# Kernel optimization log

Measured on AMD Instinct MI355X. Metric: run time of the kernel, lower is better.

## Reference

```python
import jax, jax.numpy as jnp
import numpy as np

MODES = 32
NUM_BLOCKS = 4
NUM_EXPERTS = 16
TOP_K = 4
TEMPERATURE = 2.0


def _gelu(t):
    return jax.nn.gelu(t, approximate=False)  # torch F.gelu default (erf)


def _c1(x, w, b):
    # 1x1 conv: x [B,C,H,W], w [O,C], b [O]
    return jnp.einsum('bchw,oc->bohw', x, w) + b[None, :, None, None]


def _group_norm(x, w, b, groups=8, eps=1e-5):
    B, C, H, W = x.shape
    xg = x.reshape(B, groups, C // groups, H, W)
    mu = xg.mean(axis=(2, 3, 4), keepdims=True)
    var = xg.var(axis=(2, 3, 4), keepdims=True)
    xn = ((xg - mu) * jax.lax.rsqrt(var + eps)).reshape(B, C, H, W)
    return xn * w[None, :, None, None] + b[None, :, None, None]


def _bn_eval(x, g, b, rm, rv, eps=1e-5):
    # eval-mode BatchNorm with running stats
    return (x - rm) * jax.lax.rsqrt(rv + eps) * g + b


def _afno(x, w1, b1, w2, b2):
    # x: [B,C,H,W] (channel_first). Block-diagonal complex MLP on low FFT modes.
    B, C, H, W = x.shape
    bs = C // NUM_BLOCKS
    xp = x.transpose(0, 2, 3, 1)                      # [B,H,W,C]
    xf = jnp.fft.rfft2(xp, axes=(1, 2), norm='ortho') # [B,H,Wf,C] complex64
    Wf = xf.shape[2]
    xf = xf.reshape(B, H, Wf, NUM_BLOCKS, bs)
    m = MODES
    xm = xf[:, :m, :m]                                # kept modes only
    xr, xi = xm.real, xm.imag
    o1r = _gelu(jnp.einsum('bhwni,nio->bhwno', xr, w1[0])
                - jnp.einsum('bhwni,nio->bhwno', xi, w1[1]) + b1[0])
    o1i = _gelu(jnp.einsum('bhwni,nio->bhwno', xi, w1[0])
                + jnp.einsum('bhwni,nio->bhwno', xr, w1[1]) + b1[1])
    o2r = (jnp.einsum('bhwni,nio->bhwno', o1r, w2[0])
           - jnp.einsum('bhwni,nio->bhwno', o1i, w2[1]) + b2[0])
    o2i = (jnp.einsum('bhwni,nio->bhwno', o1i, w2[0])
           + jnp.einsum('bhwni,nio->bhwno', o1r, w2[1]) + b2[1])
    of = jnp.zeros((B, H, Wf, NUM_BLOCKS, bs), dtype=xf.dtype)
    of = of.at[:, :m, :m].set(o2r + 1j * o2i)
    out = jnp.fft.irfft2(of.reshape(B, H, Wf, C), s=(H, W), axes=(1, 2), norm='ortho')
    out = out + xp
    return out.transpose(0, 3, 1, 2)


def _forward(x, gn1_w, gn1_b, afno_w1, afno_b1, afno_w2, afno_b2,
             gn2_w, gn2_b, fe_w, fe_b, g1_w, g1_b, bn1_g, bn1_b, bn1_rm, bn1_rv,
             ca_w1, ca_b1, ca_w2, ca_b2, g2_w, g2_b, bn2_g, bn2_b, bn2_rm, bn2_rv,
             g3_w, g3_b, shared_w, shared_b, expert_w, expert_b):
    residual = x
    h = _group_norm(x, gn1_w, gn1_b)
    h = _afno(h, afno_w1, afno_b1, afno_w2, afno_b2)
    h = h + residual            # double_skip
    residual = h
    h = _group_norm(h, gn2_w, gn2_b)
    # MoEImage (eval mode -> loss_gate = 0)
    feats = _gelu(_c1(h, fe_w, fe_b))
    shared = jnp.zeros_like(h)
    for s in range(shared_w.shape[0]):
        shared = shared + _gelu(_c1(feats, shared_w[s], shared_b[s])) / shared_w.shape[0]
    # gating on global-avg-pooled features (1x1 convs == linears)
    gf = feats.mean(axis=(2, 3))                              # [B,C]
    h1 = _gelu(_bn_eval(gf @ g1_w.T + g1_b, bn1_g, bn1_b, bn1_rm, bn1_rv))
    a = _gelu(h1 @ ca_w1.T + ca_b1) @ ca_w2.T + ca_b2
    h1 = h1 * jax.nn.sigmoid(2.0 * a)                          # avg==max pool on 1x1 map
    h2 = _gelu(_bn_eval(h1 @ g2_w.T + g2_b, bn2_g, bn2_b, bn2_rm, bn2_rv))
    scores = h2 @ g3_w.T + g3_b                                # [B,E]
    vals, idx = jax.lax.top_k(scores, TOP_K)
    wts = jax.nn.softmax(vals / TEMPERATURE, axis=1)
    B = x.shape[0]
    gate_w = jnp.zeros((B, NUM_EXPERTS), x.dtype).at[jnp.arange(B)[:, None], idx].add(wts)
    out = shared
    for e in range(NUM_EXPERTS):
        out = out + _gelu(_c1(feats, expert_w[e], expert_b[e])) * gate_w[:, e][:, None, None, None]
    return out + residual


def setup_inputs():
    key = jax.random.key(0)
    ks = jax.random.split(key, 16)
    B, C, H, W = 8, 64, 192, 192
    nb = NUM_BLOCKS
    bs = C // nb
    E = NUM_EXPERTS
    scale = 1.0 / (bs * bs)
    f32 = jnp.float32
    n = lambda k, shape: jax.random.normal(k, shape, f32) * 0.02
    return {
        'x': jax.random.normal(ks[0], (B, C, H, W), f32),
        'gn1_w': jnp.ones((C,), f32), 'gn1_b': jnp.zeros((C,), f32),
        'afno_w1': jax.random.uniform(ks[1], (2, nb, bs, bs), f32) * scale,
        'afno_b1': jax.random.uniform(ks[2], (2, nb, bs), f32) * scale,
        'afno_w2': jax.random.uniform(ks[3], (2, nb, bs, bs), f32) * scale,
        'afno_b2': jax.random.uniform(ks[4], (2, nb, bs), f32) * scale,
        'gn2_w': jnp.ones((C,), f32), 'gn2_b': jnp.zeros((C,), f32),
        'fe_w': n(ks[5], (C, C)), 'fe_b': jnp.zeros((C,), f32),
        'g1_w': n(ks[6], (2 * C, C)), 'g1_b': jnp.zeros((2 * C,), f32),
        'bn1_g': jnp.ones((2 * C,), f32), 'bn1_b': jnp.zeros((2 * C,), f32),
        'bn1_rm': jnp.zeros((2 * C,), f32), 'bn1_rv': jnp.ones((2 * C,), f32),
        'ca_w1': n(ks[7], (2 * C // 16, 2 * C)), 'ca_b1': jnp.zeros((2 * C // 16,), f32),
        'ca_w2': n(ks[8], (2 * C, 2 * C // 16)), 'ca_b2': jnp.zeros((2 * C,), f32),
        'g2_w': n(ks[9], (C, 2 * C)), 'g2_b': jnp.zeros((C,), f32),
        'bn2_g': jnp.ones((C,), f32), 'bn2_b': jnp.zeros((C,), f32),
        'bn2_rm': jnp.zeros((C,), f32), 'bn2_rv': jnp.ones((C,), f32),
        'g3_w': n(ks[10], (E, C)), 'g3_b': jnp.zeros((E,), f32),
        'shared_w': n(ks[11], (2, C, C)), 'shared_b': jnp.zeros((2, C), f32),
        'expert_w': n(ks[12], (E, C, C)), 'expert_b': jnp.zeros((E, C), f32),
    }


def reference(x, gn1_w, gn1_b, afno_w1, afno_b1, afno_w2, afno_b2,
              gn2_w, gn2_b, fe_w, fe_b, g1_w, g1_b, bn1_g, bn1_b, bn1_rm, bn1_rv,
              ca_w1, ca_b1, ca_w2, ca_b2, g2_w, g2_b, bn2_g, bn2_b, bn2_rm, bn2_rv,
              g3_w, g3_b, shared_w, shared_b, expert_w, expert_b):
    return _forward(x, gn1_w, gn1_b, afno_w1, afno_b1, afno_w2, afno_b2,
                    gn2_w, gn2_b, fe_w, fe_b, g1_w, g1_b, bn1_g, bn1_b, bn1_rm, bn1_rv,
                    ca_w1, ca_b1, ca_w2, ca_b2, g2_w, g2_b, bn2_g, bn2_b, bn2_rm, bn2_rv,
                    g3_w, g3_b, shared_w, shared_b, expert_w, expert_b)
```

## Files before the change

### kernel.cpp

```cpp
#include <hip/hip_runtime.h>
#include <math.h>

#define TPI 6.283185307179586f

typedef __attribute__((ext_vector_type(8))) short bf8v;
typedef __attribute__((ext_vector_type(4))) float f4v;

#define MFMA(a,b,c) __builtin_amdgcn_mfma_f32_16x16x32_bf16((a),(b),(c),0,0,0)

__device__ __forceinline__ float gelu_f(float v){
  return 0.5f*v*(1.0f+erff(v*0.7071067811865475f));
}
__device__ __forceinline__ float gelu_fast(float x){
  float x2=x*x;
  float inner=fmaf(0.044715f*x2, x, x);
  float e=__expf(1.5957691216057308f*inner);
  float r=__builtin_amdgcn_rcpf(1.0f+e);
  return fmaf(-x, r, x);
}
__device__ __forceinline__ float gelu_sig(float x){
  float e=__expf(-1.702f*x);
  return x*__builtin_amdgcn_rcpf(1.0f+e);
}
__device__ __forceinline__ unsigned short f2b(float f){
  union{float f; unsigned u;} v; v.f=f;
  unsigned r=v.u + 0x7FFFu + ((v.u>>16)&1u);
  return (unsigned short)(r>>16);
}

__global__ __launch_bounds__(256) void prep(const float* __restrict__ shw, const float* __restrict__ exw,
    const float* __restrict__ shb, const float* __restrict__ exb, const float* __restrict__ few,
    unsigned short* __restrict__ T, unsigned short* __restrict__ wall, float* __restrict__ ball,
    unsigned short* __restrict__ wfe, float* __restrict__ gfp){
  const float a = TPI/192.0f;
  int stride=gridDim.x*256;
  for(int i=blockIdx.x*256+threadIdx.x; i<61440; i+=stride){
    float v;
    if(i<12288){
      int n1=i/192, w=i%192; int kw=n1>>1, c=n1&1;
      int m=(kw*w)%192; float cs,sn; sincosf((float)m*a,&sn,&cs);
      v = c ? -sn : cs;
    } else if(i<36864){
      int j=i-12288; int n1=j/384, k1=j%384; int kh=n1>>1, d=n1&1; int h=k1>>1, c=k1&1;
      int m=(kh*h)%192; float cs,sn; sincosf((float)m*a,&sn,&cs);
      float e = d ? (c ? cs : -sn) : (c ? sn : cs);
      v = e*(1.0f/192.0f);
    } else if(i<49152){
      int j=i-36864; int h=j/64, k1=j%64; int kh=k1>>1, c=k1&1;
      int m=(h*kh)%192; float cs,sn; sincosf((float)m*a,&sn,&cs);
      v = c ? sn : cs;
    } else {
      int j=i-49152; int w=j/64, k1=j%64; int kw=k1>>1, d=k1&1;
      float f = kw ? (2.0f/192.0f) : (1.0f/192.0f);
      int m=(w*kw)%192; float cs,sn; sincosf((float)m*a,&sn,&cs);
      v = d ? -f*sn : f*cs;
    }
    T[i]=f2b(v);
  }
  for(int i=blockIdx.x*256+threadIdx.x;i<73728;i+=stride) wall[i]=f2b(i<8192?shw[i]:exw[i-8192]);
  for(int i=blockIdx.x*256+threadIdx.x;i<1152;i+=stride)  ball[i]=(i<128)?shb[i]:exb[i-128];
  for(int i=blockIdx.x*256+threadIdx.x;i<4096;i+=stride)  wfe[i]=f2b(few[i]);
  for(int i=blockIdx.x*256+threadIdx.x;i<512;i+=stride)   gfp[i]=0.f;
}

__global__ void gn_finalize(const float* __restrict__ part, const float* __restrict__ gw,
                            const float* __restrict__ gb, float2* __restrict__ sb){
  int g=threadIdx.x; if(g>=64) return;
  float S=0,SS=0;
  for(int j=0;j<8;j++){ S+=part[(g*8+j)*2]; SS+=part[(g*8+j)*2+1]; }
  const float inv=1.0f/294912.0f;
  float mean=S*inv, var=SS*inv-mean*mean;
  float rstd=rsqrtf(var+1e-5f);
  int b=g>>3, gg=g&7;
  for(int k=0;k<8;k++){
    int c=gg*8+k;
    float sc=rstd*gw[c];
    sb[b*64+c]=make_float2(sc, gb[c]-mean*sc);
  }
}

__global__ __launch_bounds__(256) void fwd_dft(const float* __restrict__ x,
      const unsigned short* __restrict__ TBf1, const unsigned short* __restrict__ TBf2,
      float* __restrict__ Xm2, float* __restrict__ part1){
  __shared__ __align__(16) unsigned short ldsA[64*200];
  __shared__ __align__(16) float sX[2048];
  __shared__ float red[8];
  int t=threadIdx.x, bc=blockIdx.x;
  int wave=t>>6, l=t&63, lr=l&15, lg=l>>4;
  const float* xch = x + (size_t)bc*36864;
  for(int i=t;i<1536;i+=256){
    int row=i/24, chunk=i%24;
    *(uint4*)&ldsA[row*200 + chunk*8] = *(const uint4*)(TBf1 + row*192 + chunk*8);
  }
  __syncthreads();
  float s_=0.f, ss_=0.f;
  f4v acc1[3][4];
  for(int mt=0;mt<3;mt++){
    int m0=(wave+mt*4)*16;
    const float* xrow = xch + (m0+lr)*192 + lg*8;
    bf8v af[6];
    #pragma unroll
    for(int ks=0;ks<6;ks++){
      float4 u0=*(const float4*)(xrow+ks*32);
      float4 u1=*(const float4*)(xrow+ks*32+4);
      s_ += u0.x+u0.y+u0.z+u0.w+u1.x+u1.y+u1.z+u1.w;
      ss_+= u0.x*u0.x+u0.y*u0.y+u0.z*u0.z+u0.w*u0.w
           +u1.x*u1.x+u1.y*u1.y+u1.z*u1.z+u1.w*u1.w;
      bf8v a;
      a[0]=(short)f2b(u0.x); a[1]=(short)f2b(u0.y); a[2]=(short)f2b(u0.z); a[3]=(short)f2b(u0.w);
      a[4]=(short)f2b(u1.x); a[5]=(short)f2b(u1.y); a[6]=(short)f2b(u1.z); a[7]=(short)f2b(u1.w);
      af[ks]=a;
    }
    #pragma unroll
    for(int nt=0;nt<4;nt++){
      f4v acc={0.f,0.f,0.f,0.f};
      #pragma unroll
      for(int ks=0;ks<6;ks++){
        bf8v b=*(const bf8v*)&ldsA[(nt*16+lr)*200 + ks*32 + lg*8];
        acc=MFMA(af[ks],b,acc);
      }
      acc1[mt][nt]=acc;
    }
  }
  __syncthreads();
  for(int mt=0;mt<3;mt++){
    int m0=(wave+mt*4)*16;
    #pragma unroll
    for(int nt=0;nt<4;nt++){
      int n1=nt*16+lr; int kw=n1>>1, c=n1&1;
      #pragma unroll
      for(int reg=0;reg<4;reg++){
        int h=m0+4*lg+reg;
        ldsA[kw*392 + 2*h + c]=f2b(acc1[mt][nt][reg]);
      }
    }
  }
  __syncthreads();
  for(int pp=0;pp<2;pp++){
    int p=wave+pp*4;
    int m0=(p>>2)*16, n0=(p&3)*16;
    f4v acc={0.f,0.f,0.f,0.f};
    #pragma unroll
    for(int ks=0;ks<12;ks++){
      bf8v a=*(const bf8v*)&ldsA[(m0+lr)*392 + ks*32 + lg*8];
      bf8v b=*(const bf8v*)(TBf2 + (n0+lr)*384 + ks*32 + lg*8);
      acc=MFMA(a,b,acc);
    }
    int n1=n0+lr; int kh=n1>>1, d=n1&1;
    #pragma unroll
    for(int reg=0;reg<4;reg++){
      int kw=m0+4*lg+reg;
      sX[(kh*32+kw)*2 + d]=acc[reg];
    }
  }
  __syncthreads();
  float* dst=Xm2+(size_t)bc*2048;
  for(int i=t;i<512;i+=256) *(float4*)(dst+i*4)=*(const float4*)(sX+i*4);
  #pragma unroll
  for(int o=32;o>0;o>>=1){ s_+=__shfl_down(s_,o); ss_+=__shfl_down(ss_,o); }
  if(l==0){ red[wave]=s_; red[4+wave]=ss_; }
  __syncthreads();
  if(t==0){
    part1[bc*2]  =red[0]+red[1]+red[2]+red[3];
    part1[bc*2+1]=red[4]+red[5]+red[6]+red[7];
  }
}

__global__ __launch_bounds__(256) void mode_mlp(const float* __restrict__ Xm2, const float2* __restrict__ sb1,
    const float* __restrict__ w1, const float* __restrict__ b1,
    const float* __restrict__ w2, const float* __restrict__ b2,
    float* __restrict__ S2){
  __shared__ float w10[1024], w11[1024], w20[1024], w21[1024];
  __shared__ float b10[64], b11[64], b20[64], b21[64];
  __shared__ float2 sbl[64];
  __shared__ float xr[32][64], xi[32][64];
  __shared__ float o1r[32][64], o1i[32][64];
  int t=threadIdx.x;
  int b=blockIdx.x>>5, kh=blockIdx.x&31;
  for(int i=t;i<1024;i+=256){ w10[i]=w1[i]; w11[i]=w1[1024+i]; w20[i]=w2[i]; w21[i]=w2[1024+i]; }
  if(t<64){ b10[t]=b1[t]; b11[t]=b1[64+t]; b20[t]=b2[t]; b21[t]=b2[64+t]; sbl[t]=sb1[b*64+t]; }
  __syncthreads();
  for(int q=0;q<16;q++){
    int idx=q*256+t; int c=idx>>6, jj=idx&63;
    float2 s=sbl[c];
    float v=Xm2[((size_t)(b*64+c))*2048 + kh*64 + jj]*s.x;
    if(kh==0 && jj==0) v += 192.0f*s.y;
    if(jj&1) xi[jj>>1][c]=v; else xr[jj>>1][c]=v;
  }
  __syncthreads();
  int tl=t&63, n=tl>>4, o=tl&15, wb=n*256+o;
  #pragma unroll
  for(int it=0;it<8;it++){
    int kw=(t>>6)+it*4;
    float a_r=b10[tl], a_i=b11[tl];
    #pragma unroll
    for(int i=0;i<16;i++){
      float rr=xr[kw][n*16+i], im=xi[kw][n*16+i];
      float W0=w10[wb+i*16], W1=w11[wb+i*16];
      a_r=fmaf(rr,W0,fmaf(-im,W1,a_r));
      a_i=fmaf(im,W0,fmaf( rr,W1,a_i));
    }
    o1r[kw][tl]=gelu_f(a_r); o1i[kw][tl]=gelu_f(a_i);
  }
  __syncthreads();
  #pragma unroll
  for(int it=0;it<8;it++){
    int kw=(t>>6)+it*4;
    float c_r=b20[tl], c_i=b21[tl];
    #pragma unroll
    for(int i=0;i<16;i++){
      float rr=o1r[kw][n*16+i], im=o1i[kw][n*16+i];
      float W0=w20[wb+i*16], W1=w21[wb+i*16];
      c_r=fmaf(rr,W0,fmaf(-im,W1,c_r));
      c_i=fmaf(im,W0,fmaf( rr,W1,c_i));
    }
    xr[kw][tl]=c_r; xi[kw][tl]=c_i;
  }
  __syncthreads();
  for(int q=0;q<16;q++){
    int idx=q*256+t; int c=idx>>6, jj=idx&63;
    float v = (jj&1) ? xi[jj>>1][c] : xr[jj>>1][c];
    S2[((size_t)(b*64+c))*2048 + kh*64 + jj]=v;
  }
}

__global__ __launch_bounds__(256) void inv_dft(const float* __restrict__ S2,
      const unsigned short* __restrict__ TAi, const unsigned short* __restrict__ TBi,
      const float* __restrict__ x, const float2* __restrict__ sb,
      float* __restrict__ h2, float* __restrict__ part2){
  __shared__ __align__(16) unsigned short Bs[64*72];
  __shared__ __align__(16) unsigned short GL[192*72];
  __shared__ float red[8];
  int t=threadIdx.x, bc=blockIdx.x;
  int wave=t>>6, l=t&63, lr=l&15, lg=l>>4;
  const float* sp=S2+(size_t)bc*2048;
  for(int i=t;i<1024;i+=256){
    int kh=i>>5, kw=i&31;
    float Sr=sp[(kh*32+kw)*2], Si=sp[(kh*32+kw)*2+1];
    unsigned short br=f2b(Sr), bi_=f2b(Si), nbi=f2b(-Si);
    Bs[(2*kw+0)*72 + 2*kh+0]=br;
    Bs[(2*kw+0)*72 + 2*kh+1]=nbi;
    Bs[(2*kw+1)*72 + 2*kh+0]=bi_;
    Bs[(2*kw+1)*72 + 2*kh+1]=br;
  }
  __syncthreads();
  for(int mt=0;mt<3;mt++){
    int m0=(wave+mt*4)*16;
    bf8v a0=*(const bf8v*)(TAi + (m0+lr)*64 + lg*8);
    bf8v a1=*(const bf8v*)(TAi + (m0+lr)*64 + 32 + lg*8);
    #pragma unroll
    for(int nt=0;nt<4;nt++){
      f4v acc={0.f,0.f,0.f,0.f};
      bf8v b0=*(const bf8v*)&Bs[(nt*16+lr)*72 + lg*8];
      bf8v b1=*(const bf8v*)&Bs[(nt*16+lr)*72 + 32 + lg*8];
      acc=MFMA(a0,b0,acc); acc=MFMA(a1,b1,acc);
      #pragma unroll
      for(int reg=0;reg<4;reg++)
        GL[(m0+4*lg+reg)*72 + nt*16+lr]=f2b(acc[reg]);
    }
  }
  __syncthreads();
  float2 sv=sb[bc];
  float cA=sv.x+1.0f, cB=sv.y;
  asm volatile("" : "+v"(cA), "+v"(cB));
  const float* xch=x+(size_t)bc*36864;
  float* och=h2+(size_t)bc*36864;
  float s_=0.f, ss_=0.f;
  for(int mt=0;mt<3;mt++){
    int m0=(wave+mt*4)*16;
    bf8v a0=*(const bf8v*)&GL[(m0+lr)*72 + lg*8];
    bf8v a1=*(const bf8v*)&GL[(m0+lr)*72 + 32 + lg*8];
    for(int nt=0;nt<12;nt++){
      int n0=nt*16;
      f4v acc={0.f,0.f,0.f,0.f};
      bf8v b0=*(const bf8v*)(TBi + (n0+lr)*64 + lg*8);
      bf8v b1=*(const bf8v*)(TBi + (n0+lr)*64 + 32 + lg*8);
      acc=MFMA(a0,b0,acc); acc=MFMA(a1,b1,acc);
      int w=n0+lr;
      #pragma unroll
      for(int reg=0;reg<4;reg++){
        int h=m0+4*lg+reg;
        int ga=h*192+w;
        float xv=xch[ga];
        float val=acc[reg]+fmaf(cA,xv,cB);
        och[ga]=val;
        s_+=val; ss_+=val*val;
      }
    }
  }
  #pragma unroll
  for(int o=32;o>0;o>>=1){ s_+=__shfl_down(s_,o); ss_+=__shfl_down(ss_,o); }
  if(l==0){ red[wave]=s_; red[4+wave]=ss_; }
  __syncthreads();
  if(t==0){
    part2[bc*2]  =red[0]+red[1]+red[2]+red[3];
    part2[bc*2+1]=red[4]+red[5]+red[6]+red[7];
  }
}

__global__ __launch_bounds__(256,4) void gf_k(const float* __restrict__ h2, const float2* __restrict__ sb,
    const unsigned short* __restrict__ wfe, const float* __restrict__ feb,
    float* __restrict__ gfp, unsigned short* __restrict__ feats){
  __shared__ __align__(16) unsigned short A[128*72];
  __shared__ float sgf[64];
  int t=threadIdx.x;
  int blk=blockIdx.x, b=blk/288, tile=blk-b*288, hw0=tile*128;
  if(t<64) sgf[t]=0.f;
  float4 v[8];
  #pragma unroll
  for(int k=0;k<8;k++){
    int i=t+k*256; int c=i>>5, q=i&31;
    v[k]=*(const float4*)&h2[(size_t)(b*64+c)*36864 + hw0 + q*4];
  }
  #pragma unroll
  for(int k=0;k<8;k++){
    int i=t+k*256; int c=i>>5, q=i&31;
    float2 s=sb[b*64+c];
    int px0=q*4, sw=((px0>>4)&3)<<3, cc=c^sw;
    A[(px0+0)*72+cc]=f2b(fmaf(v[k].x,s.x,s.y));
    A[(px0+1)*72+cc]=f2b(fmaf(v[k].y,s.x,s.y));
    A[(px0+2)*72+cc]=f2b(fmaf(v[k].z,s.x,s.y));
    A[(px0+3)*72+cc]=f2b(fmaf(v[k].w,s.x,s.y));
  }
  __syncthreads();
  int wave=t>>6, l=t&63, lr=l&15, lg=l>>4;
  int pxb=wave*32;
  bf8v af[2][2];
  #pragma unroll
  for(int fm=0;fm<2;fm++){
    int row=pxb+fm*16+lr, sw=((row>>4)&3)<<3;
    #pragma unroll
    for(int ks=0;ks<2;ks++) af[fm][ks]=*(const bf8v*)&A[row*72+((ks*32+lg*8)^sw)];
  }
  float gsum[4]={0.f,0.f,0.f,0.f};
  #pragma unroll
  for(int fn=0;fn<4;fn++){
    bf8v b0=*(const bf8v*)(wfe+(fn*16+lr)*64+lg*8);
    bf8v b1=*(const bf8v*)(wfe+(fn*16+lr)*64+32+lg*8);
    float bs=feb[fn*16+lr];
    #pragma unroll
    for(int fm=0;fm<2;fm++){
      f4v acc={0.f,0.f,0.f,0.f};
      acc=MFMA(af[fm][0],b0,acc);
      acc=MFMA(af[fm][1],b1,acc);
      int swm=(((pxb+fm*16)>>4)&3)<<3;
      int cc=(fn*16+lr)^swm;
      #pragma unroll
      for(int r=0;r<4;r++){
        float g=gelu_fast(acc[r]+bs);
        gsum[fn]+=g;
        A[(pxb+fm*16+4*lg+r)*72+cc]=f2b(g);
      }
    }
  }
  #pragma unroll
  for(int fn=0;fn<4;fn++){
    float v2=gsum[fn];
    v2+=__shfl_xor(v2,16); v2+=__shfl_xor(v2,32);
    if(lg==0) atomicAdd(&sgf[fn*16+lr], v2);
  }
  __syncthreads();
  if(t<64) atomicAdd(&gfp[b*64+t], sgf[t]);
  #pragma unroll
  for(int k=0;k<4;k++){
    int i=t+k*256; int px=i>>3, c0=(i&7)*8, sw=((px>>4)&3)<<3;
    *(uint4*)&feats[(size_t)(b*36864+hw0+px)*64+c0] = *(const uint4*)&A[px*72+(c0^sw)];
  }
}

__global__ __launch_bounds__(128) void gating(const float* __restrict__ gfp,
  const float* __restrict__ g1w, const float* __restrict__ g1b,
  const float* __restrict__ bn1g, const float* __restrict__ bn1b, const float* __restrict__ bn1m, const float* __restrict__ bn1v,
  const float* __restrict__ cw1, const float* __restrict__ cb1, const float* __restrict__ cw2, const float* __restrict__ cb2,
  const float* __restrict__ g2w, const float* __restrict__ g2b,
  const float* __restrict__ bn2g, const float* __restrict__ bn2b, const float* __restrict__ bn2m, const float* __restrict__ bn2v,
  const float* __restrict__ g3w, const float* __restrict__ g3b, float2* __restrict__ act){
  __shared__ float gf[8][64];
  __shared__ float h1[8][128];
  __shared__ float a1[8][8];
  __shared__ float h2g[8][64];
  __shared__ float sc[8][16];
  int t=threadIdx.x;
  for(int i=t;i<512;i+=128) gf[i>>6][i&63]=gfp[i]*(1.0f/36864.0f);
  __syncthreads();
  for(int i=t;i<1024;i+=128){
    int b=i>>7, j=i&127;
    float s=g1b[j];
    for(int c=0;c<64;c++) s=fmaf(gf[b][c], g1w[j*64+c], s);
    s=(s-bn1m[j])*rsqrtf(bn1v[j]+1e-5f)*bn1g[j]+bn1b[j];
    h1[b][j]=gelu_f(s);
  }
  __syncthreads();
  if(t<64){
    int b=t>>3, k=t&7; float s=cb1[k];
    for(int j=0;j<128;j++) s=fmaf(h1[b][j], cw1[k*128+j], s);
    a1[b][k]=gelu_f(s);
  }
  __syncthreads();
  for(int i=t;i<1024;i+=128){
    int b=i>>7, j=i&127;
    float s=cb2[j];
    for(int k=0;k<8;k++) s=fmaf(a1[b][k], cw2[j*8+k], s);
    h1[b][j]=h1[b][j]/(1.0f+expf(-2.0f*s));
  }
  __syncthreads();
  for(int i=t;i<512;i+=128){
    int b=i>>6, j=i&63;
    float s=g2b[j];
    for(int k=0;k<128;k++) s=fmaf(h1[b][k], g2w[j*128+k], s);
    s=(s-bn2m[j])*rsqrtf(bn2v[j]+1e-5f)*bn2g[j]+bn2b[j];
    h2g[b][j]=gelu_f(s);
  }
  __syncthreads();
  {
    int b=t>>4, e=t&15;
    float s=g3b[e];
    for(int c=0;c<64;c++) s=fmaf(h2g[b][c], g3w[e*64+c], s);
    sc[b][e]=s;
  }
  __syncthreads();
  if(t<8){
    int b=t;
    float v[16];
    for(int e=0;e<16;e++) v[e]=sc[b][e];
    float vals[4]; int idx[4];
    for(int k=0;k<4;k++){
      float best=-1e30f; int bi=0;
      for(int e=0;e<16;e++) if(v[e]>best){best=v[e];bi=e;}
      vals[k]=best; idx[k]=bi; v[bi]=-1e30f;
    }
    float m=vals[0], ssum=0.f, w[4];
    for(int k=0;k<4;k++){ w[k]=expf((vals[k]-m)*0.5f); ssum+=w[k]; }
    act[b*6+0]=make_float2(0.5f, __int_as_float(0));
    act[b*6+1]=make_float2(0.5f, __int_as_float(1));
    for(int k=0;k<4;k++) act[b*6+2+k]=make_float2(w[k]/ssum, __int_as_float(2+idx[k]));
  }
}

__global__ __launch_bounds__(256,4) void final_k(const unsigned short* __restrict__ feats,
  const unsigned short* __restrict__ wall, const float* __restrict__ ball,
  const float2* __restrict__ act, float* __restrict__ out){
  __shared__ __align__(16) unsigned short A[128*72];
  int t=threadIdx.x;
  int blk=blockIdx.x, b=blk/288, tile=blk-b*288, hw0=tile*128;
  uint4 fv[4];
  #pragma unroll
  for(int k=0;k<4;k++){
    int i=t+k*256; int px=i>>3, c0=(i&7)*8;
    fv[k]=*(const uint4*)&feats[(size_t)(b*36864+hw0+px)*64+c0];
  }
  #pragma unroll
  for(int k=0;k<4;k++){
    int i=t+k*256; int px=i>>3, c0=(i&7)*8, sw=((px>>4)&3)<<3;
    *(uint4*)&A[px*72+(c0^sw)]=fv[k];
  }
  __syncthreads();
  int wave=t>>6, l=t&63, lr=l&15, lg=l>>4;
  int pxb=wave*32;
  bf8v af2[2][2];
  #pragma unroll
  for(int fm=0;fm<2;fm++){
    int row=pxb+fm*16+lr, sw=((row>>4)&3)<<3;
    #pragma unroll
    for(int ks=0;ks<2;ks++) af2[fm][ks]=*(const bf8v*)&A[row*72+((ks*32+lg*8)^sw)];
  }
  float* Fo=(float*)A;
  #pragma unroll
  for(int half=0;half<2;half++){
    float oa[2][2][4]={};
    for(int j=0;j<6;j++){
      float2 aw=act[b*6+j];
      int term=__float_as_int(aw.y);
      float g=aw.x;
      const unsigned short* wp=wall+term*4096;
      const float* bp=ball+term*64;
      #pragma unroll
      for(int fn2=0;fn2<2;fn2++){
        int fn=half*2+fn2;
        bf8v b0=*(const bf8v*)(wp+(fn*16+lr)*64+lg*8);
        bf8v b1=*(const bf8v*)(wp+(fn*16+lr)*64+32+lg*8);
        float bs=bp[fn*16+lr];
        #pragma unroll
        for(int fm=0;fm<2;fm++){
          f4v acc={0.f,0.f,0.f,0.f};
          acc=MFMA(af2[fm][0],b0,acc);
          acc=MFMA(af2[fm][1],b1,acc);
          #pragma unroll
          for(int r=0;r<4;r++)
            oa[fm][fn2][r]=fmaf(g, gelu_sig(acc[r]+bs), oa[fm][fn2][r]);
        }
      }
    }
    __syncthreads();
    #pragma unroll
    for(int fm=0;fm<2;fm++)
      #pragma unroll
      for(int fn2=0;fn2<2;fn2++){
        int ocl=fn2*16+lr;
        *(float4*)&Fo[ocl*132 + pxb + fm*16 + 4*lg] =
            make_float4(oa[fm][fn2][0],oa[fm][fn2][1],oa[fm][fn2][2],oa[fm][fn2][3]);
      }
    __syncthreads();
    for(int i=t;i<1024;i+=256){
      int ocl=i>>5, px0=(i&31)*4;
      int oc=half*32+ocl;
      size_t base=(size_t)(b*64+oc)*36864 + hw0 + px0;
      float4 rv=*(const float4*)&out[base];
      float4 ov=*(const float4*)&Fo[ocl*132+px0];
      *(float4*)&out[base]=make_float4(ov.x+rv.x,ov.y+rv.y,ov.z+rv.z,ov.w+rv.w);
    }
  }
}

extern "C" void kernel_launch(void* const* d_in, const int* in_sizes, int n_in,
                              void* d_out, int out_size, void* d_ws, size_t ws_size,
                              hipStream_t stream){
  const float* x    =(const float*)d_in[0];
  const float* gn1w =(const float*)d_in[1];
  const float* gn1b =(const float*)d_in[2];
  const float* aw1  =(const float*)d_in[3];
  const float* ab1  =(const float*)d_in[4];
  const float* aw2  =(const float*)d_in[5];
  const float* ab2  =(const float*)d_in[6];
  const float* gn2w =(const float*)d_in[7];
  const float* gn2b =(const float*)d_in[8];
  const float* few  =(const float*)d_in[9];
  const float* feb  =(const float*)d_in[10];
  const float* g1w  =(const float*)d_in[11];
  const float* g1b  =(const float*)d_in[12];
  const float* bn1g =(const float*)d_in[13];
  const float* bn1b =(const float*)d_in[14];
  const float* bn1m =(const float*)d_in[15];
  const float* bn1v =(const float*)d_in[16];
  const float* cw1  =(const float*)d_in[17];
  const float* cb1  =(const float*)d_in[18];
  const float* cw2  =(const float*)d_in[19];
  const float* cb2  =(const float*)d_in[20];
  const float* g2w  =(const float*)d_in[21];
  const float* g2b  =(const float*)d_in[22];
  const float* bn2g =(const float*)d_in[23];
  const float* bn2b =(const float*)d_in[24];
  const float* bn2m =(const float*)d_in[25];
  const float* bn2v =(const float*)d_in[26];
  const float* g3w  =(const float*)d_in[27];
  const float* g3b  =(const float*)d_in[28];
  const float* shw  =(const float*)d_in[29];
  const float* shb  =(const float*)d_in[30];
  const float* exw  =(const float*)d_in[31];
  const float* exb  =(const float*)d_in[32];

  float* out=(float*)d_out;
  float* ws=(float*)d_ws;

  float*  part1 = ws;
  float*  part2 = ws+1024;
  float2* sb1   = (float2*)(ws+2048);
  float2* sb2   = (float2*)(ws+3072);
  float2* act   = (float2*)(ws+4096);
  float*  gfp   = ws+4224;
  float*  Xm2   = ws+8192;
  float*  S2    = ws+1056768;
  unsigned short* Tbl  = (unsigned short*)(ws+2105344);
  unsigned short* wall = (unsigned short*)(ws+2136064);
  float*          ball = ws+2172928;
  unsigned short* wfe  = (unsigned short*)(ws+2174080);
  unsigned short* feats= (unsigned short*)(ws+2176128);
  const unsigned short* TBf1 = Tbl;
  const unsigned short* TBf2 = Tbl+12288;
  const unsigned short* TAi  = Tbl+36864;
  const unsigned short* TBi  = Tbl+49152;

  prep<<<64,256,0,stream>>>(shw, exw, shb, exb, few, Tbl, wall, ball, wfe, gfp);
  fwd_dft <<<512,256,0,stream>>>(x, TBf1, TBf2, Xm2, part1);
  gn_finalize<<<1,64,0,stream>>>(part1, gn1w, gn1b, sb1);
  mode_mlp<<<256,256,0,stream>>>(Xm2, sb1, aw1, ab1, aw2, ab2, S2);
  inv_dft <<<512,256,0,stream>>>(S2, TAi, TBi, x, sb1, out, part2);
  gn_finalize<<<1,64,0,stream>>>(part2, gn2w, gn2b, sb2);
  gf_k<<<2304,256,0,stream>>>(out, sb2, wfe, feb, gfp, feats);
  gating <<<1,128,0,stream>>>(gfp, g1w,g1b, bn1g,bn1b,bn1m,bn1v,
                              cw1,cb1,cw2,cb2, g2w,g2b, bn2g,bn2b,bn2m,bn2v,
                              g3w,g3b, act);
  final_k<<<2304,256,0,stream>>>(feats, wall, ball, act, out);
}
```

Before: 210.7 us.

## Make gf_k and final_k persistent over three tiles with register prefetch

Both per-pixel kernels now launch 768 blocks, and each block loops over three 128-pixel tiles. The next tile's input is loaded into registers while the current tile is computed, so global load latency overlaps with the MFMA and GELU work. In final_k the residual read of out is also issued before the expert loop rather than after it. The cost is fewer resident blocks per GPU, higher register pressure from the prefetch buffers, and extra barriers.

```diff
diff --git a/kernel.cpp b/kernel.cpp
--- a/kernel.cpp
+++ b/kernel.cpp
@@ -304,67 +304,81 @@
   __shared__ __align__(16) unsigned short A[128*72];
   __shared__ float sgf[64];
   int t=threadIdx.x;
-  int blk=blockIdx.x, b=blk/288, tile=blk-b*288, hw0=tile*128;
-  if(t<64) sgf[t]=0.f;
-  float4 v[8];
-  #pragma unroll
-  for(int k=0;k<8;k++){
-    int i=t+k*256; int c=i>>5, q=i&31;
-    v[k]=*(const float4*)&h2[(size_t)(b*64+c)*36864 + hw0 + q*4];
-  }
-  #pragma unroll
-  for(int k=0;k<8;k++){
-    int i=t+k*256; int c=i>>5, q=i&31;
-    float2 s=sb[b*64+c];
-    int px0=q*4, sw=((px0>>4)&3)<<3, cc=c^sw;
-    A[(px0+0)*72+cc]=f2b(fmaf(v[k].x,s.x,s.y));
-    A[(px0+1)*72+cc]=f2b(fmaf(v[k].y,s.x,s.y));
-    A[(px0+2)*72+cc]=f2b(fmaf(v[k].z,s.x,s.y));
-    A[(px0+3)*72+cc]=f2b(fmaf(v[k].w,s.x,s.y));
-  }
-  __syncthreads();
   int wave=t>>6, l=t&63, lr=l&15, lg=l>>4;
   int pxb=wave*32;
-  bf8v af[2][2];
-  #pragma unroll
-  for(int fm=0;fm<2;fm++){
-    int row=pxb+fm*16+lr, sw=((row>>4)&3)<<3;
-    #pragma unroll
-    for(int ks=0;ks<2;ks++) af[fm][ks]=*(const bf8v*)&A[row*72+((ks*32+lg*8)^sw)];
-  }
-  float gsum[4]={0.f,0.f,0.f,0.f};
-  #pragma unroll
-  for(int fn=0;fn<4;fn++){
-    bf8v b0=*(const bf8v*)(wfe+(fn*16+lr)*64+lg*8);
-    bf8v b1=*(const bf8v*)(wfe+(fn*16+lr)*64+32+lg*8);
-    float bs=feb[fn*16+lr];
+  float4 v[8];
+  {
+    int blk=blockIdx.x, b=blk/288, tile=blk-b*288, hw0=tile*128;
+    #pragma unroll
+    for(int k=0;k<8;k++){
+      int i=t+k*256; int c=i>>5, q=i&31;
+      v[k]=*(const float4*)&h2[(size_t)(b*64+c)*36864 + hw0 + q*4];
+    }
+  }
+  for(int it=0;it<3;it++){
+    int blk=blockIdx.x+it*768, b=blk/288, tile=blk-b*288, hw0=tile*128;
+    __syncthreads();
+    if(t<64) sgf[t]=0.f;
+    #pragma unroll
+    for(int k=0;k<8;k++){
+      int i=t+k*256; int c=i>>5, q=i&31;
+      float2 s=sb[b*64+c];
+      int px0=q*4, sw=((px0>>4)&3)<<3, cc=c^sw;
+      A[(px0+0)*72+cc]=f2b(fmaf(v[k].x,s.x,s.y));
+      A[(px0+1)*72+cc]=f2b(fmaf(v[k].y,s.x,s.y));
+      A[(px0+2)*72+cc]=f2b(fmaf(v[k].z,s.x,s.y));
+      A[(px0+3)*72+cc]=f2b(fmaf(v[k].w,s.x,s.y));
+    }
+    __syncthreads();
+    bf8v af[2][2];
     #pragma unroll
     for(int fm=0;fm<2;fm++){
-      f4v acc={0.f,0.f,0.f,0.f};
-      acc=MFMA(af[fm][0],b0,acc);
-      acc=MFMA(af[fm][1],b1,acc);
-      int swm=(((pxb+fm*16)>>4)&3)<<3;
-      int cc=(fn*16+lr)^swm;
-      #pragma unroll
-      for(int r=0;r<4;r++){
-        float g=gelu_fast(acc[r]+bs);
-        gsum[fn]+=g;
-        A[(pxb+fm*16+4*lg+r)*72+cc]=f2b(g);
-      }
-    }
-  }
-  #pragma unroll
-  for(int fn=0;fn<4;fn++){
-    float v2=gsum[fn];
-    v2+=__shfl_xor(v2,16); v2+=__shfl_xor(v2,32);
-    if(lg==0) atomicAdd(&sgf[fn*16+lr], v2);
-  }
-  __syncthreads();
-  if(t<64) atomicAdd(&gfp[b*64+t], sgf[t]);
-  #pragma unroll
-  for(int k=0;k<4;k++){
-    int i=t+k*256; int px=i>>3, c0=(i&7)*8, sw=((px>>4)&3)<<3;
-    *(uint4*)&feats[(size_t)(b*36864+hw0+px)*64+c0] = *(const uint4*)&A[px*72+(c0^sw)];
+      int row=pxb+fm*16+lr, sw=((row>>4)&3)<<3;
+      #pragma unroll
+      for(int ks=0;ks<2;ks++) af[fm][ks]=*(const bf8v*)&A[row*72+((ks*32+lg*8)^sw)];
+    }
+    if(it<2){
+      int nblk=blockIdx.x+(it+1)*768, nb=nblk/288, ntile=nblk-nb*288, nhw0=ntile*128;
+      #pragma unroll
+      for(int k=0;k<8;k++){
+        int i=t+k*256; int c=i>>5, q=i&31;
+        v[k]=*(const float4*)&h2[(size_t)(nb*64+c)*36864 + nhw0 + q*4];
+      }
+    }
+    float gsum[4]={0.f,0.f,0.f,0.f};
+    #pragma unroll
+    for(int fn=0;fn<4;fn++){
+      bf8v b0=*(const bf8v*)(wfe+(fn*16+lr)*64+lg*8);
+      bf8v b1=*(const bf8v*)(wfe+(fn*16+lr)*64+32+lg*8);
+      float bs=feb[fn*16+lr];
+      #pragma unroll
+      for(int fm=0;fm<2;fm++){
+        f4v acc={0.f,0.f,0.f,0.f};
+        acc=MFMA(af[fm][0],b0,acc);
+        acc=MFMA(af[fm][1],b1,acc);
+        int swm=(((pxb+fm*16)>>4)&3)<<3;
+        int cc=(fn*16+lr)^swm;
+        #pragma unroll
+        for(int r=0;r<4;r++){
+          float g=gelu_fast(acc[r]+bs);
+          gsum[fn]+=g;
+          A[(pxb+fm*16+4*lg+r)*72+cc]=f2b(g);
+        }
+      }
+    }
+    #pragma unroll
+    for(int fn=0;fn<4;fn++){
+      float v2=gsum[fn];
+      v2+=__shfl_xor(v2,16); v2+=__shfl_xor(v2,32);
+      if(lg==0) atomicAdd(&sgf[fn*16+lr], v2);
+    }
+    __syncthreads();
+    if(t<64) atomicAdd(&gfp[b*64+t], sgf[t]);
+    #pragma unroll
+    for(int k=0;k<4;k++){
+      int i=t+k*256; int px=i>>3, c0=(i&7)*8, sw=((px>>4)&3)<<3;
+      *(uint4*)&feats[(size_t)(b*36864+hw0+px)*64+c0] = *(const uint4*)&A[px*72+(c0^sw)];
+    }
   }
 }
 
@@ -442,72 +456,92 @@
   const float2* __restrict__ act, float* __restrict__ out){
   __shared__ __align__(16) unsigned short A[128*72];
   int t=threadIdx.x;
-  int blk=blockIdx.x, b=blk/288, tile=blk-b*288, hw0=tile*128;
-  uint4 fv[4];
-  #pragma unroll
-  for(int k=0;k<4;k++){
-    int i=t+k*256; int px=i>>3, c0=(i&7)*8;
-    fv[k]=*(const uint4*)&feats[(size_t)(b*36864+hw0+px)*64+c0];
-  }
-  #pragma unroll
-  for(int k=0;k<4;k++){
-    int i=t+k*256; int px=i>>3, c0=(i&7)*8, sw=((px>>4)&3)<<3;
-    *(uint4*)&A[px*72+(c0^sw)]=fv[k];
-  }
-  __syncthreads();
   int wave=t>>6, l=t&63, lr=l&15, lg=l>>4;
   int pxb=wave*32;
-  bf8v af2[2][2];
-  #pragma unroll
-  for(int fm=0;fm<2;fm++){
-    int row=pxb+fm*16+lr, sw=((row>>4)&3)<<3;
-    #pragma unroll
-    for(int ks=0;ks<2;ks++) af2[fm][ks]=*(const bf8v*)&A[row*72+((ks*32+lg*8)^sw)];
-  }
-  float* Fo=(float*)A;
-  #pragma unroll
-  for(int half=0;half<2;half++){
-    float oa[2][2][4]={};
-    for(int j=0;j<6;j++){
-      float2 aw=act[b*6+j];
-      int term=__float_as_int(aw.y);
-      float g=aw.x;
-      const unsigned short* wp=wall+term*4096;
-      const float* bp=ball+term*64;
-      #pragma unroll
-      for(int fn2=0;fn2<2;fn2++){
-        int fn=half*2+fn2;
-        bf8v b0=*(const bf8v*)(wp+(fn*16+lr)*64+lg*8);
-        bf8v b1=*(const bf8v*)(wp+(fn*16+lr)*64+32+lg*8);
-        float bs=bp[fn*16+lr];
+  uint4 fv[4];
+  {
+    int blk=blockIdx.x, b=blk/288, tile=blk-b*288, hw0=tile*128;
+    #pragma unroll
+    for(int k=0;k<4;k++){
+      int i=t+k*256; int px=i>>3, c0=(i&7)*8;
+      fv[k]=*(const uint4*)&feats[(size_t)(b*36864+hw0+px)*64+c0];
+    }
+  }
+  for(int it=0;it<3;it++){
+    int blk=blockIdx.x+it*768, b=blk/288, tile=blk-b*288, hw0=tile*128;
+    __syncthreads();
+    #pragma unroll
+    for(int k=0;k<4;k++){
+      int i=t+k*256; int px=i>>3, c0=(i&7)*8, sw=((px>>4)&3)<<3;
+      *(uint4*)&A[px*72+(c0^sw)]=fv[k];
+    }
+    __syncthreads();
+    bf8v af2[2][2];
+    #pragma unroll
+    for(int fm=0;fm<2;fm++){
+      int row=pxb+fm*16+lr, sw=((row>>4)&3)<<3;
+      #pragma unroll
+      for(int ks=0;ks<2;ks++) af2[fm][ks]=*(const bf8v*)&A[row*72+((ks*32+lg*8)^sw)];
+    }
+    if(it<2){
+      int nblk=blockIdx.x+(it+1)*768, nb=nblk/288, ntile=nblk-nb*288, nhw0=ntile*128;
+      #pragma unroll
+      for(int k=0;k<4;k++){
+        int i=t+k*256; int px=i>>3, c0=(i&7)*8;
+        fv[k]=*(const uint4*)&feats[(size_t)(nb*36864+nhw0+px)*64+c0];
+      }
+    }
+    float* Fo=(float*)A;
+    #pragma unroll
+    for(int half=0;half<2;half++){
+      float4 rv[4];
+      #pragma unroll
+      for(int k2=0;k2<4;k2++){
+        int i=t+k2*256; int ocl=i>>5, px0=(i&31)*4, oc=half*32+ocl;
+        rv[k2]=*(const float4*)&out[(size_t)(b*64+oc)*36864 + hw0 + px0];
+      }
+      float oa[2][2][4]={};
+      for(int j=0;j<6;j++){
+        float2 aw=act[b*6+j];
+        int term=__float_as_int(aw.y);
+        float g=aw.x;
+        const unsigned short* wp=wall+term*4096;
+        const float* bp=ball+term*64;
         #pragma unroll
-        for(int fm=0;fm<2;fm++){
-          f4v acc={0.f,0.f,0.f,0.f};
-          acc=MFMA(af2[fm][0],b0,acc);
-          acc=MFMA(af2[fm][1],b1,acc);
+        for(int fn2=0;fn2<2;fn2++){
+          int fn=half*2+fn2;
+          bf8v b0=*(const bf8v*)(wp+(fn*16+lr)*64+lg*8);
+          bf8v b1=*(const bf8v*)(wp+(fn*16+lr)*64+32+lg*8);
+          float bs=bp[fn*16+lr];
           #pragma unroll
-          for(int r=0;r<4;r++)
-            oa[fm][fn2][r]=fmaf(g, gelu_sig(acc[r]+bs), oa[fm][fn2][r]);
+          for(int fm=0;fm<2;fm++){
+            f4v acc={0.f,0.f,0.f,0.f};
+            acc=MFMA(af2[fm][0],b0,acc);
+            acc=MFMA(af2[fm][1],b1,acc);
+            #pragma unroll
+            for(int r=0;r<4;r++)
+              oa[fm][fn2][r]=fmaf(g, gelu_sig(acc[r]+bs), oa[fm][fn2][r]);
+          }
         }
       }
-    }
-    __syncthreads();
-    #pragma unroll
-    for(int fm=0;fm<2;fm++)
-      #pragma unroll
-      for(int fn2=0;fn2<2;fn2++){
-        int ocl=fn2*16+lr;
-        *(float4*)&Fo[ocl*132 + pxb + fm*16 + 4*lg] =
-            make_float4(oa[fm][fn2][0],oa[fm][fn2][1],oa[fm][fn2][2],oa[fm][fn2][3]);
-      }
-    __syncthreads();
-    for(int i=t;i<1024;i+=256){
-      int ocl=i>>5, px0=(i&31)*4;
-      int oc=half*32+ocl;
-      size_t base=(size_t)(b*64+oc)*36864 + hw0 + px0;
-      float4 rv=*(const float4*)&out[base];
-      float4 ov=*(const float4*)&Fo[ocl*132+px0];
-      *(float4*)&out[base]=make_float4(ov.x+rv.x,ov.y+rv.y,ov.z+rv.z,ov.w+rv.w);
+      __syncthreads();
+      #pragma unroll
+      for(int fm=0;fm<2;fm++)
+        #pragma unroll
+        for(int fn2=0;fn2<2;fn2++){
+          int ocl=fn2*16+lr;
+          *(float4*)&Fo[ocl*132 + pxb + fm*16 + 4*lg] =
+              make_float4(oa[fm][fn2][0],oa[fm][fn2][1],oa[fm][fn2][2],oa[fm][fn2][3]);
+        }
+      __syncthreads();
+      #pragma unroll
+      for(int k2=0;k2<4;k2++){
+        int i=t+k2*256; int ocl=i>>5, px0=(i&31)*4, oc=half*32+ocl;
+        size_t base=(size_t)(b*64+oc)*36864 + hw0 + px0;
+        float4 ov=*(const float4*)&Fo[ocl*132+px0];
+        *(float4*)&out[base]=make_float4(ov.x+rv[k2].x,ov.y+rv[k2].y,
+                                         ov.z+rv[k2].z,ov.w+rv[k2].w);
+      }
     }
   }
 }
@@ -576,9 +610,9 @@
   mode_mlp<<<256,256,0,stream>>>(Xm2, sb1, aw1, ab1, aw2, ab2, S2);
   inv_dft <<<512,256,0,stream>>>(S2, TAi, TBi, x, sb1, out, part2);
   gn_finalize<<<1,64,0,stream>>>(part2, gn2w, gn2b, sb2);
-  gf_k<<<2304,256,0,stream>>>(out, sb2, wfe, feb, gfp, feats);
+  gf_k<<<768,256,0,stream>>>(out, sb2, wfe, feb, gfp, feats);
   gating <<<1,128,0,stream>>>(gfp, g1w,g1b, bn1g,bn1b,bn1m,bn1v,
                               cw1,cb1,cw2,cb2, g2w,g2b, bn2g,bn2b,bn2m,bn2v,
                               g3w,g3b, act);
-  final_k<<<2304,256,0,stream>>>(feats, wall, ball, act, out);
-}
+  final_k<<<768,256,0,stream>>>(feats, wall, ball, act, out);
+}
```

After: 265.3 us. 25.9% more time.
